# Kernel optimization log

Hardware: AMD Instinct MI355X
Metric: run time of the kernel (lower is better)

The kernel has to match this reference:

```python
import jax, jax.numpy as jnp
import numpy as np

B, T, D, H = 4, 2048, 1024, 16
HD = D // H  # head_dim = 64


def setup_inputs() -> dict:
    key = jax.random.key(0)
    k1, k2, k3, k4, k5 = jax.random.split(key, 5)
    scale = 1.0 / np.sqrt(D)
    return {
        "x": jax.random.normal(k1, (B, T, D), dtype=jnp.float32),
        "mask": jnp.ones((B, T), dtype=jnp.int32),
        "W_qkv": jax.random.normal(k2, (D, 3 * D), dtype=jnp.float32) * scale,
        "b_qkv": jax.random.normal(k3, (3 * D,), dtype=jnp.float32) * 0.01,
        "W_out": jax.random.normal(k4, (D, D), dtype=jnp.float32) * scale,
        "b_out": jax.random.normal(k5, (D,), dtype=jnp.float32) * 0.01,
    }


def reference(x, mask, W_qkv, b_qkv, W_out, b_out):
    Bx, Tx, Dm = x.shape
    qkv = x @ W_qkv + b_qkv                      # [B,T,3D]
    qkv = qkv.reshape(Bx, Tx, 3, H, HD)
    qkv = jnp.transpose(qkv, (2, 0, 3, 1, 4))    # [3,B,H,T,hd]
    q, k, v = qkv[0], qkv[1], qkv[2]
    att = jnp.einsum("bhqd,bhkd->bhqk", q, k) / jnp.sqrt(jnp.float32(HD))
    m = (mask[:, None, None, :] == 0)            # [B,1,1,T]
    att = jnp.where(m, jnp.float32(-1e9), att)
    att = jax.nn.softmax(att, axis=-1)
    out = jnp.einsum("bhqk,bhkd->bhqd", att, v)  # [B,H,T,hd]
    out = jnp.transpose(out, (0, 2, 1, 3)).reshape(Bx, Tx, Dm)
    return out @ W_out + b_out
```

## Files before the change

kernel.cpp:

```cpp
#include <hip/hip_runtime.h>
#include <hip/hip_bf16.h>
#include <stdint.h>

#define B_  4
#define T_  2048
#define D_  1024
#define H_  16
#define HD_ 64

typedef short s16x8 __attribute__((ext_vector_type(8)));
typedef short s16x4 __attribute__((ext_vector_type(4)));
typedef float f32x4 __attribute__((ext_vector_type(4)));

#define MFMA32(a, b, c) __builtin_amdgcn_mfma_f32_16x16x32_bf16(a, b, c, 0, 0, 0)

#if __has_builtin(__builtin_amdgcn_exp2f)
#define FEXP2(x) __builtin_amdgcn_exp2f(x)
#else
#define FEXP2(x) exp2f(x)
#endif

__device__ __forceinline__ unsigned short f2bf(float f) {
    union { float f; unsigned int u; } v; v.f = f;
    unsigned int r = v.u + 0x7fffu + ((v.u >> 16) & 1u);
    return (unsigned short)(r >> 16);
}

__device__ __forceinline__ unsigned int pkbf(float a, float b) {
    __hip_bfloat162 h = __float22bfloat162_rn(float2{a, b});
    union { __hip_bfloat162 h; unsigned int u; } v; v.h = h;
    return v.u;
}

__device__ __forceinline__ void async16(const void* g, void* l) {
    __builtin_amdgcn_global_load_lds(
        (const __attribute__((address_space(1))) unsigned int*)g,
        (__attribute__((address_space(3))) unsigned int*)l, 16, 0, 0);
}

__global__ __launch_bounds__(256)
void prep_kernel(const float* __restrict__ x, unsigned short* __restrict__ xb,
                 const float* __restrict__ Wq, unsigned short* __restrict__ Wqt,
                 const float* __restrict__ Wo, unsigned short* __restrict__ Wot) {
    const int blk = blockIdx.x;
    const int tid = threadIdx.x;
    if (blk < 8192) {
        const int i = blk * 256 + tid;
        float4 v = ((const float4*)x)[i];
        ushort4 o;
        o.x = f2bf(v.x); o.y = f2bf(v.y); o.z = f2bf(v.z); o.w = f2bf(v.w);
        ((ushort4*)xb)[i] = o;
        return;
    }
    __shared__ float t[32][33];
    const float* W; unsigned short* Wt; int K, N, bx, by;
    if (blk < 11264) {
        const int idx = blk - 8192;
        W = Wq; Wt = Wqt; K = 1024; N = 3072;
        bx = (idx % 96) * 32; by = (idx / 96) * 32;
    } else {
        const int idx = blk - 11264;
        W = Wo; Wt = Wot; K = 1024; N = 1024;
        bx = (idx % 32) * 32; by = (idx / 32) * 32;
    }
    const int tx = tid & 31, ty = tid >> 5;
    #pragma unroll
    for (int j = 0; j < 32; j += 8)
        t[ty + j][tx] = W[(size_t)(by + ty + j) * N + bx + tx];
    __syncthreads();
    #pragma unroll
    for (int j = 0; j < 32; j += 8)
        Wt[(size_t)(bx + ty + j) * K + by + tx] = f2bf(t[tx][ty + j]);
}

template <int MODE>
__global__ __launch_bounds__(256)
void gemm_bt_kernel(const unsigned short* __restrict__ A,
                    const unsigned short* __restrict__ Bt,
                    const float* __restrict__ bias,
                    float* __restrict__ Cf,
                    unsigned short* __restrict__ Qo,
                    unsigned short* __restrict__ Ko,
                    unsigned short* __restrict__ Vo,
                    int M, int N, int K) {
    __shared__ __align__(16) unsigned short SMEM[4 * 128 * 64];
    const int tid = threadIdx.x;
    const int w = tid >> 6, lane = tid & 63;
    const int laneN = lane & 15, quad = lane >> 4;
    const int rm0 = blockIdx.x * 128;
    const int rn0 = blockIdx.y * 128;
    const int wr = (w >> 1) * 64, wc = (w & 1) * 64;

    f32x4 acc[4][4] = {};

    auto issueG = [&](int kk, int bufsel) {
        unsigned short* As = SMEM + bufsel * 8192;
        unsigned short* Bs = SMEM + 16384 + bufsel * 8192;
        #pragma unroll
        for (int i = 0; i < 4; ++i) {
            const int c = i * 256 + tid;
            const int row = c >> 3, s = c & 7, g = s ^ (row & 7);
            async16(A + (size_t)(rm0 + row) * K + kk + g * 8,
                    (char*)As + (size_t)c * 16);
        }
        #pragma unroll
        for (int i = 0; i < 4; ++i) {
            const int c = i * 256 + tid;
            const int row = c >> 3, s = c & 7, g = s ^ (row & 7);
            async16(Bt + (size_t)(rn0 + row) * K + kk + g * 8,
                    (char*)Bs + (size_t)c * 16);
        }
    };

    issueG(0, 0);
    const int KI = K >> 6;
    for (int it = 0; it < KI; ++it) {
        const int buf = it & 1;
        __syncthreads();
        const unsigned short* As = SMEM + buf * 8192;
        const unsigned short* Bs = SMEM + 16384 + buf * 8192;
        s16x8 av[2][4], bv[2][4];
        #pragma unroll
        for (int h = 0; h < 2; ++h) {
            #pragma unroll
            for (int ms = 0; ms < 4; ++ms) {
                const int row = wr + ms * 16 + laneN;
                av[h][ms] = *(const s16x8*)&As[row * 64 + ((h * 4 + quad) ^ (row & 7)) * 8];
            }
            #pragma unroll
            for (int ns = 0; ns < 4; ++ns) {
                const int row = wc + ns * 16 + laneN;
                bv[h][ns] = *(const s16x8*)&Bs[row * 64 + ((h * 4 + quad) ^ (row & 7)) * 8];
            }
        }
        if (it + 1 < KI) issueG((it + 1) << 6, buf ^ 1);
        #pragma unroll
        for (int ms = 0; ms < 4; ++ms)
            #pragma unroll
            for (int ns = 0; ns < 4; ++ns) {
                acc[ms][ns] = MFMA32(av[0][ms], bv[0][ns], acc[ms][ns]);
                acc[ms][ns] = MFMA32(av[1][ms], bv[1][ns], acc[ms][ns]);
            }
    }

    if (MODE == 0) {
        #pragma unroll
        for (int ms = 0; ms < 4; ++ms) {
            const int gm0 = rm0 + wr + ms * 16 + quad * 4;
            #pragma unroll
            for (int ns = 0; ns < 4; ++ns) {
                const int gn = rn0 + wc + ns * 16 + laneN;
                const float bb = bias[gn];
                #pragma unroll
                for (int r = 0; r < 4; ++r)
                    Cf[(size_t)(gm0 + r) * N + gn] = acc[ms][ns][r] + bb;
            }
        }
    } else {
        const int s = rn0 >> 10;
        const int bidx = rm0 >> 11, t0 = rm0 & (T_ - 1);
        if (s < 2) {
            const float fs = (s == 0) ? 0.125f * 1.44269504088896f : 1.0f;
            unsigned short* P = (s == 0) ? Qo : Ko;
            #pragma unroll
            for (int ms = 0; ms < 4; ++ms) {
                const int lm0 = wr + ms * 16 + quad * 4;
                #pragma unroll
                for (int ns = 0; ns < 4; ++ns) {
                    const int gn = rn0 + wc + ns * 16 + laneN;
                    const float bb = bias[gn];
                    const int rr = gn & 1023, hh = rr >> 6, dd = rr & 63;
                    const size_t base = ((size_t)(bidx * H_ + hh) * T_ + t0);
                    #pragma unroll
                    for (int r = 0; r < 4; ++r)
                        P[(base + lm0 + r) * HD_ + dd] =
                            f2bf((acc[ms][ns][r] + bb) * fs);
                }
            }
        } else {
            __syncthreads();
            #pragma unroll
            for (int ms = 0; ms < 4; ++ms) {
                const int lm0 = wr + ms * 16 + quad * 4;
                #pragma unroll
                for (int ns = 0; ns < 4; ++ns) {
                    const int nl = wc + ns * 16 + laneN;
                    const float bb = bias[rn0 + nl];
                    const int sw = (nl & 7) << 3;
                    #pragma unroll
                    for (int r = 0; r < 4; ++r)
                        SMEM[nl * 128 + ((lm0 + r) ^ sw)] =
                            f2bf(acc[ms][ns][r] + bb);
                }
            }
            __syncthreads();
            const int nl = tid >> 1, half = tid & 1;
            const int hh = nl >> 6, d = nl & 63;
            const int hAbs = bidx * H_ + ((rn0 & 1023) >> 6) + hh;
            unsigned short* rowp = Vo + ((size_t)hAbs * HD_ + d) * T_ + t0;
            const int swz = nl & 7;
            #pragma unroll
            for (int j = 0; j < 8; ++j) {
                const s16x8 vv = *(const s16x8*)&SMEM[nl * 128 + half * 64 + j * 8];
                const int mlog = half * 64 + ((j ^ swz) * 8);
                *(s16x8*)(rowp + mlog) = vv;
            }
        }
    }
}

__global__ __launch_bounds__(512, 4)
void attn_kernel(const unsigned short* __restrict__ Q,
                 const unsigned short* __restrict__ Kb,
                 const unsigned short* __restrict__ VT,
                 const int* __restrict__ mask,
                 unsigned short* __restrict__ Out) {
    __shared__ __align__(16) unsigned short Ks[2][64 * 64];
    __shared__ __align__(16) unsigned short Vs[2][64 * 64];
    __shared__ float biasF[T_];
    const int tid = threadIdx.x;
    const int lane = tid & 63;
    const int w = tid >> 6;
    const int laneN = lane & 15, quad = lane >> 4;
    const int x7 = laneN & 7;
    const int bh = blockIdx.x;
    const int b = bh >> 4, h = bh & 15;
    const int qbase = blockIdx.y * 256 + w * 32;

    for (int i = tid; i < T_; i += 512)
        biasF[i] = mask[b * T_ + i] ? 0.f : -1.0e9f;

    s16x8 qf[2][2];
    #pragma unroll
    for (int qg = 0; qg < 2; ++qg) {
        const size_t qoff = ((size_t)bh * T_ + qbase + qg * 16 + laneN) * HD_ + quad * 8;
        qf[qg][0] = *(const s16x8*)&Q[qoff];
        qf[qg][1] = *(const s16x8*)&Q[qoff + 32];
    }

    s16x8 ones;
    #pragma unroll
    for (int j = 0; j < 8; ++j) ones[j] = (short)0x3F80;

    const size_t kRow0 = (size_t)bh * T_ * HD_;
    const size_t vRow0 = (size_t)bh * HD_ * T_;

    auto issueTile = [&](int kt, int bufsel) {
        const int kbase = kt * 64;
        {
            const int c = tid;
            const int row = c >> 3, s = c & 7;
            const int fk = (row & 3) | (((row >> 3) & 1) << 2);
            const int g = s ^ fk;
            async16(Kb + kRow0 + (size_t)(kbase + row) * HD_ + g * 8,
                    &Ks[bufsel][c * 8]);
        }
        {
            const int c = tid;
            const int d = c >> 3, s = c & 7, g = s ^ (d & 7);
            async16(VT + vRow0 + (size_t)d * T_ + kbase + g * 8,
                    &Vs[bufsel][c * 8]);
        }
    };

    issueTile(0, 0);

    f32x4 O[2][4] = {};
    f32x4 liacc[2] = {};

    const int rowA = ((laneN >> 2) << 3) + (laneN & 3);

    #pragma unroll 2
    for (int kt = 0; kt < T_ / 64; ++kt) {
        const int buf = kt & 1;
        const int kbase = kt * 64;
        __syncthreads();
        if (kt + 1 < T_ / 64) issueTile(kt + 1, buf ^ 1);

        s16x8 pf[2][2];
        #pragma unroll
        for (int g32 = 0; g32 < 2; ++g32) {
            const int ra = g32 * 32 + rowA;
            const s16x8 kA0 = *(const s16x8*)&Ks[buf][(ra * 8 + (quad ^ x7)) * 8];
            const s16x8 kA1 = *(const s16x8*)&Ks[buf][(ra * 8 + ((4 + quad) ^ x7)) * 8];
            const s16x8 kB0 = *(const s16x8*)&Ks[buf][((ra + 4) * 8 + (quad ^ x7)) * 8];
            const s16x8 kB1 = *(const s16x8*)&Ks[buf][((ra + 4) * 8 + ((4 + quad) ^ x7)) * 8];
            const f32x4 bA = *(const f32x4*)&biasF[kbase + g32 * 32 + quad * 8];
            const f32x4 bB = *(const f32x4*)&biasF[kbase + g32 * 32 + quad * 8 + 4];
            #pragma unroll
            for (int qg = 0; qg < 2; ++qg) {
                f32x4 Sa = bA, Sb = bB;
                Sa = MFMA32(kA0, qf[qg][0], Sa);
                Sa = MFMA32(kA1, qf[qg][1], Sa);
                Sb = MFMA32(kB0, qf[qg][0], Sb);
                Sb = MFMA32(kB1, qf[qg][1], Sb);
                #pragma unroll
                for (int r = 0; r < 4; ++r) {
                    Sa[r] = FEXP2(Sa[r]);
                    Sb[r] = FEXP2(Sb[r]);
                }
                union { s16x8 v; unsigned int u[4]; } pu;
                pu.u[0] = pkbf(Sa[0], Sa[1]);
                pu.u[1] = pkbf(Sa[2], Sa[3]);
                pu.u[2] = pkbf(Sb[0], Sb[1]);
                pu.u[3] = pkbf(Sb[2], Sb[3]);
                pf[qg][g32] = pu.v;
            }
        }

        #pragma unroll
        for (int g32 = 0; g32 < 2; ++g32) {
            s16x8 vf[4];
            #pragma unroll
            for (int nt = 0; nt < 4; ++nt) {
                const int d = nt * 16 + laneN;
                vf[nt] = *(const s16x8*)&Vs[buf][(d * 8 + ((g32 * 4 + quad) ^ x7)) * 8];
            }
            #pragma unroll
            for (int qg = 0; qg < 2; ++qg) {
                #pragma unroll
                for (int nt = 0; nt < 4; ++nt)
                    O[qg][nt] = MFMA32(pf[qg][g32], vf[nt], O[qg][nt]);
                liacc[qg] = MFMA32(pf[qg][g32], ones, liacc[qg]);
            }
        }
    }

    #pragma unroll
    for (int qg = 0; qg < 2; ++qg) {
        #pragma unroll
        for (int r = 0; r < 4; ++r) {
            const float inv = 1.0f / liacc[qg][r];
            const int tq = qbase + qg * 16 + quad * 4 + r;
            #pragma unroll
            for (int nt = 0; nt < 4; ++nt)
                Out[(size_t)(b * T_ + tq) * D_ + h * HD_ + nt * 16 + laneN] =
                    f2bf(O[qg][nt][r] * inv);
        }
    }
}

extern "C" void kernel_launch(void* const* d_in, const int* in_sizes, int n_in,
                              void* d_out, int out_size, void* d_ws, size_t ws_size,
                              hipStream_t stream) {
    const float* x     = (const float*)d_in[0];
    const int*   mask  = (const int*)d_in[1];
    const float* W_qkv = (const float*)d_in[2];
    const float* b_qkv = (const float*)d_in[3];
    const float* W_out = (const float*)d_in[4];
    const float* b_out = (const float*)d_in[5];
    float* out = (float*)d_out;

    unsigned short* ws = (unsigned short*)d_ws;
    const size_t NX = (size_t)B_ * T_ * D_;
    unsigned short* xb  = ws;
    unsigned short* Qb  = xb + NX;
    unsigned short* Kb  = Qb + NX;
    unsigned short* Vtb = Kb + NX;
    unsigned short* Wqt = Vtb + NX;
    unsigned short* Wot = Wqt + (size_t)3 * D_ * D_;
    unsigned short* attn = xb;

    prep_kernel<<<12288, 256, 0, stream>>>(x, xb, W_qkv, Wqt, W_out, Wot);
    gemm_bt_kernel<1><<<dim3(B_ * T_ / 128, 3 * D_ / 128), 256, 0, stream>>>(
        xb, Wqt, b_qkv, nullptr, Qb, Kb, Vtb, B_ * T_, 3 * D_, D_);
    attn_kernel<<<dim3(B_ * H_, T_ / 256), 512, 0, stream>>>(Qb, Kb, Vtb, mask, attn);
    gemm_bt_kernel<0><<<dim3(B_ * T_ / 128, D_ / 128), 256, 0, stream>>>(
        attn, Wot, b_out, out, nullptr, nullptr, nullptr, B_ * T_, D_, D_);
}
```

Baseline: 247.3 us.

## Add 256x256-tile QKV GEMM kernel with 512 threads and double-buffered async loads

Replaces the 128x128-tile QKV projection GEMM with a dedicated kernel using 256x256 output tiles, 8 waves, swizzled LDS double-buffering via async global-to-LDS copies, and setprio around MFMA bursts. Larger tiles raise arithmetic intensity and cut global/L2 traffic per FLOP. The V-transpose epilogue is adapted to the wider tile. In exchange it uses 128KB LDS and many accumulator registers per block, which lowers occupancy, and the grid shrinks to 384 blocks, which may under-fill the GPU.

```diff
diff --git a/kernel.cpp b/kernel.cpp
--- a/kernel.cpp
+++ b/kernel.cpp
@@ -156,55 +156,153 @@
                     Cf[(size_t)(gm0 + r) * N + gn] = acc[ms][ns][r] + bb;
             }
         }
+    }
+}
+
+__global__ __launch_bounds__(512, 2)
+void gemm256_qkv_kernel(const unsigned short* __restrict__ A,
+                        const unsigned short* __restrict__ Bt,
+                        const float* __restrict__ bias,
+                        unsigned short* __restrict__ Qo,
+                        unsigned short* __restrict__ Ko,
+                        unsigned short* __restrict__ Vo,
+                        int M, int N, int K) {
+    __shared__ __align__(16) unsigned short SMEM[65536];
+    const int tid = threadIdx.x;
+    const int w = tid >> 6, lane = tid & 63;
+    const int laneN = lane & 15, quad = lane >> 4;
+    const int wm = w >> 2, wn = w & 3;
+    const int rm0 = blockIdx.x * 256;
+    const int rn0 = blockIdx.y * 256;
+
+    f32x4 acc[8][4] = {};
+
+    auto issueTile = [&](int kk, int bufsel) {
+        unsigned short* As = SMEM + bufsel * 16384;
+        unsigned short* Bs = SMEM + 32768 + bufsel * 16384;
+        #pragma unroll
+        for (int i = 0; i < 4; ++i) {
+            const int c = i * 512 + tid;
+            const int row = c >> 3, s = c & 7, g = s ^ (row & 7);
+            async16(A + (size_t)(rm0 + row) * K + kk + g * 8,
+                    (char*)As + (size_t)c * 16);
+        }
+        #pragma unroll
+        for (int i = 0; i < 4; ++i) {
+            const int c = i * 512 + tid;
+            const int row = c >> 3, s = c & 7, g = s ^ (row & 7);
+            async16(Bt + (size_t)(rn0 + row) * K + kk + g * 8,
+                    (char*)Bs + (size_t)c * 16);
+        }
+    };
+
+    issueTile(0, 0);
+    issueTile(64, 1);
+    asm volatile("s_waitcnt vmcnt(8)" ::: "memory");
+    __builtin_amdgcn_s_barrier();
+    asm volatile("" ::: "memory");
+
+    const int KI = K >> 6;
+    #pragma unroll 2
+    for (int kt = 0; kt < KI; ++kt) {
+        const int buf = kt & 1;
+        const unsigned short* As = SMEM + buf * 16384;
+        const unsigned short* Bs = SMEM + 32768 + buf * 16384;
+        s16x8 av[4], bv[4];
+        #pragma unroll
+        for (int kh = 0; kh < 2; ++kh) {
+            #pragma unroll
+            for (int ns = 0; ns < 4; ++ns) {
+                const int row = wn * 64 + ns * 16 + laneN;
+                bv[ns] = *(const s16x8*)&Bs[row * 64 + ((kh * 4 + quad) ^ (row & 7)) * 8];
+            }
+            #pragma unroll
+            for (int ms = 0; ms < 4; ++ms) {
+                const int row = wm * 128 + ms * 16 + laneN;
+                av[ms] = *(const s16x8*)&As[row * 64 + ((kh * 4 + quad) ^ (row & 7)) * 8];
+            }
+            __builtin_amdgcn_s_setprio(1);
+            #pragma unroll
+            for (int ms = 0; ms < 4; ++ms)
+                #pragma unroll
+                for (int ns = 0; ns < 4; ++ns)
+                    acc[ms][ns] = MFMA32(av[ms], bv[ns], acc[ms][ns]);
+            __builtin_amdgcn_s_setprio(0);
+            #pragma unroll
+            for (int ms = 0; ms < 4; ++ms) {
+                const int row = wm * 128 + 64 + ms * 16 + laneN;
+                av[ms] = *(const s16x8*)&As[row * 64 + ((kh * 4 + quad) ^ (row & 7)) * 8];
+            }
+            __builtin_amdgcn_s_setprio(1);
+            #pragma unroll
+            for (int ms = 0; ms < 4; ++ms)
+                #pragma unroll
+                for (int ns = 0; ns < 4; ++ns)
+                    acc[4 + ms][ns] = MFMA32(av[ms], bv[ns], acc[4 + ms][ns]);
+            __builtin_amdgcn_s_setprio(0);
+        }
+        __builtin_amdgcn_s_barrier();
+        asm volatile("" ::: "memory");
+        if (kt + 2 < KI) {
+            issueTile((kt + 2) << 6, buf);
+            asm volatile("s_waitcnt vmcnt(8)" ::: "memory");
+        } else if (kt + 1 < KI) {
+            asm volatile("s_waitcnt vmcnt(0)" ::: "memory");
+        }
+        if (kt + 1 < KI) {
+            __builtin_amdgcn_s_barrier();
+            asm volatile("" ::: "memory");
+        }
+    }
+
+    const int s = rn0 >> 10;
+    const int bidx = rm0 >> 11, t0 = rm0 & (T_ - 1);
+    if (s < 2) {
+        const float fs = (s == 0) ? 0.125f * 1.44269504088896f : 1.0f;
+        unsigned short* P = (s == 0) ? Qo : Ko;
+        #pragma unroll
+        for (int a = 0; a < 8; ++a) {
+            const int lm0 = wm * 128 + (a >> 2) * 64 + (a & 3) * 16 + quad * 4;
+            #pragma unroll
+            for (int ns = 0; ns < 4; ++ns) {
+                const int gn = rn0 + wn * 64 + ns * 16 + laneN;
+                const float bb = bias[gn];
+                const int rr = gn & 1023, hh = rr >> 6, dd = rr & 63;
+                const size_t base = ((size_t)(bidx * H_ + hh) * T_ + t0);
+                #pragma unroll
+                for (int r = 0; r < 4; ++r)
+                    P[(base + lm0 + r) * HD_ + dd] =
+                        f2bf((acc[a][ns][r] + bb) * fs);
+            }
+        }
     } else {
-        const int s = rn0 >> 10;
-        const int bidx = rm0 >> 11, t0 = rm0 & (T_ - 1);
-        if (s < 2) {
-            const float fs = (s == 0) ? 0.125f * 1.44269504088896f : 1.0f;
-            unsigned short* P = (s == 0) ? Qo : Ko;
-            #pragma unroll
-            for (int ms = 0; ms < 4; ++ms) {
-                const int lm0 = wr + ms * 16 + quad * 4;
-                #pragma unroll
-                for (int ns = 0; ns < 4; ++ns) {
-                    const int gn = rn0 + wc + ns * 16 + laneN;
-                    const float bb = bias[gn];
-                    const int rr = gn & 1023, hh = rr >> 6, dd = rr & 63;
-                    const size_t base = ((size_t)(bidx * H_ + hh) * T_ + t0);
-                    #pragma unroll
-                    for (int r = 0; r < 4; ++r)
-                        P[(base + lm0 + r) * HD_ + dd] =
-                            f2bf((acc[ms][ns][r] + bb) * fs);
-                }
-            }
-        } else {
-            __syncthreads();
-            #pragma unroll
-            for (int ms = 0; ms < 4; ++ms) {
-                const int lm0 = wr + ms * 16 + quad * 4;
-                #pragma unroll
-                for (int ns = 0; ns < 4; ++ns) {
-                    const int nl = wc + ns * 16 + laneN;
-                    const float bb = bias[rn0 + nl];
-                    const int sw = (nl & 7) << 3;
-                    #pragma unroll
-                    for (int r = 0; r < 4; ++r)
-                        SMEM[nl * 128 + ((lm0 + r) ^ sw)] =
-                            f2bf(acc[ms][ns][r] + bb);
-                }
-            }
-            __syncthreads();
-            const int nl = tid >> 1, half = tid & 1;
-            const int hh = nl >> 6, d = nl & 63;
-            const int hAbs = bidx * H_ + ((rn0 & 1023) >> 6) + hh;
-            unsigned short* rowp = Vo + ((size_t)hAbs * HD_ + d) * T_ + t0;
-            const int swz = nl & 7;
-            #pragma unroll
-            for (int j = 0; j < 8; ++j) {
-                const s16x8 vv = *(const s16x8*)&SMEM[nl * 128 + half * 64 + j * 8];
-                const int mlog = half * 64 + ((j ^ swz) * 8);
-                *(s16x8*)(rowp + mlog) = vv;
-            }
+        __syncthreads();
+        #pragma unroll
+        for (int a = 0; a < 8; ++a) {
+            const int lm0 = wm * 128 + (a >> 2) * 64 + (a & 3) * 16 + quad * 4;
+            #pragma unroll
+            for (int ns = 0; ns < 4; ++ns) {
+                const int nl = wn * 64 + ns * 16 + laneN;
+                const float bb = bias[rn0 + nl];
+                const int sw = (nl & 7) << 3;
+                #pragma unroll
+                for (int r = 0; r < 4; ++r)
+                    SMEM[nl * 256 + ((lm0 + r) ^ sw)] =
+                        f2bf(acc[a][ns][r] + bb);
+            }
+        }
+        __syncthreads();
+        const int nl = tid >> 1, half = tid & 1;
+        const int hh = nl >> 6, d = nl & 63;
+        const int hAbs = bidx * H_ + ((rn0 & 1023) >> 6) + hh;
+        unsigned short* rowp = Vo + ((size_t)hAbs * HD_ + d) * T_ + t0;
+        const int swz = nl & 7;
+        #pragma unroll
+        for (int j = 0; j < 16; ++j) {
+            const int mgl = half * 16 + j;
+            const int pg = (mgl & 24) | ((mgl & 7) ^ swz);
+            const s16x8 vv = *(const s16x8*)&SMEM[nl * 256 + pg * 8];
+            *(s16x8*)(rowp + mgl * 8) = vv;
         }
     }
 }
@@ -362,8 +460,8 @@
     unsigned short* attn = xb;
 
     prep_kernel<<<12288, 256, 0, stream>>>(x, xb, W_qkv, Wqt, W_out, Wot);
-    gemm_bt_kernel<1><<<dim3(B_ * T_ / 128, 3 * D_ / 128), 256, 0, stream>>>(
-        xb, Wqt, b_qkv, nullptr, Qb, Kb, Vtb, B_ * T_, 3 * D_, D_);
+    gemm256_qkv_kernel<<<dim3(B_ * T_ / 256, 3 * D_ / 256), 512, 0, stream>>>(
+        xb, Wqt, b_qkv, Qb, Kb, Vtb, B_ * T_, 3 * D_, D_);
     attn_kernel<<<dim3(B_ * H_, T_ / 256), 512, 0, stream>>>(Qb, Kb, Vtb, mask, attn);
     gemm_bt_kernel<0><<<dim3(B_ * T_ / 128, D_ / 128), 256, 0, stream>>>(
         attn, Wot, b_out, out, nullptr, nullptr, nullptr, B_ * T_, D_, D_);
```

Measured after the change: 264.0 us. 6.8% more time.

## Use 128-key tiles, fuse QK and PV per chunk, add MFMA priority hints

Applied to the files above, without the earlier changes.

Doubles the K/V tile per iteration from 64 to 128 keys, which halves the number of __syncthreads barriers and async-copy rounds. The QK^T, exp and PV stages are merged per 32-key chunk, so P fragments are consumed right away instead of being buffered. s_setprio is raised around the MFMA groups to favour matrix issue across waves. Doubled LDS (about 72KB per block) may lower occupancy against the launch bound of 4 blocks, and the V swizzle changes to a 16-slot layout.

```diff
diff --git a/kernel.cpp b/kernel.cpp
--- a/kernel.cpp
+++ b/kernel.cpp
@@ -215,8 +215,8 @@
                  const unsigned short* __restrict__ VT,
                  const int* __restrict__ mask,
                  unsigned short* __restrict__ Out) {
-    __shared__ __align__(16) unsigned short Ks[2][64 * 64];
-    __shared__ __align__(16) unsigned short Vs[2][64 * 64];
+    __shared__ __align__(16) unsigned short Ks[2][128 * 64];
+    __shared__ __align__(16) unsigned short Vs[2][64 * 128];
     __shared__ float biasF[T_];
     const int tid = threadIdx.x;
     const int lane = tid & 63;
@@ -246,18 +246,21 @@
     const size_t vRow0 = (size_t)bh * HD_ * T_;
 
     auto issueTile = [&](int kt, int bufsel) {
-        const int kbase = kt * 64;
-        {
-            const int c = tid;
+        const int kbase = kt * 128;
+        #pragma unroll
+        for (int i = 0; i < 2; ++i) {
+            const int c = i * 512 + tid;
             const int row = c >> 3, s = c & 7;
             const int fk = (row & 3) | (((row >> 3) & 1) << 2);
             const int g = s ^ fk;
             async16(Kb + kRow0 + (size_t)(kbase + row) * HD_ + g * 8,
                     &Ks[bufsel][c * 8]);
         }
-        {
-            const int c = tid;
-            const int d = c >> 3, s = c & 7, g = s ^ (d & 7);
+        #pragma unroll
+        for (int i = 0; i < 2; ++i) {
+            const int c = i * 512 + tid;
+            const int d = c >> 4, s = c & 15;
+            const int g = (s & 8) | ((s & 7) ^ (d & 7));
             async16(VT + vRow0 + (size_t)d * T_ + kbase + g * 8,
                     &Vs[bufsel][c * 8]);
         }
@@ -270,30 +273,39 @@
 
     const int rowA = ((laneN >> 2) << 3) + (laneN & 3);
 
+    const int NT = T_ / 128;
     #pragma unroll 2
-    for (int kt = 0; kt < T_ / 64; ++kt) {
+    for (int kt = 0; kt < NT; ++kt) {
         const int buf = kt & 1;
-        const int kbase = kt * 64;
+        const int kbase = kt * 128;
         __syncthreads();
-        if (kt + 1 < T_ / 64) issueTile(kt + 1, buf ^ 1);
-
-        s16x8 pf[2][2];
-        #pragma unroll
-        for (int g32 = 0; g32 < 2; ++g32) {
+        if (kt + 1 < NT) issueTile(kt + 1, buf ^ 1);
+
+        #pragma unroll
+        for (int g32 = 0; g32 < 4; ++g32) {
             const int ra = g32 * 32 + rowA;
             const s16x8 kA0 = *(const s16x8*)&Ks[buf][(ra * 8 + (quad ^ x7)) * 8];
             const s16x8 kA1 = *(const s16x8*)&Ks[buf][(ra * 8 + ((4 + quad) ^ x7)) * 8];
             const s16x8 kB0 = *(const s16x8*)&Ks[buf][((ra + 4) * 8 + (quad ^ x7)) * 8];
             const s16x8 kB1 = *(const s16x8*)&Ks[buf][((ra + 4) * 8 + ((4 + quad) ^ x7)) * 8];
+            s16x8 vf[4];
+            const int jslot = g32 * 4 + quad;
+            #pragma unroll
+            for (int nt = 0; nt < 4; ++nt) {
+                const int d = nt * 16 + laneN;
+                vf[nt] = *(const s16x8*)&Vs[buf][(d * 16 + (jslot ^ x7)) * 8];
+            }
             const f32x4 bA = *(const f32x4*)&biasF[kbase + g32 * 32 + quad * 8];
             const f32x4 bB = *(const f32x4*)&biasF[kbase + g32 * 32 + quad * 8 + 4];
             #pragma unroll
             for (int qg = 0; qg < 2; ++qg) {
                 f32x4 Sa = bA, Sb = bB;
+                __builtin_amdgcn_s_setprio(1);
                 Sa = MFMA32(kA0, qf[qg][0], Sa);
                 Sa = MFMA32(kA1, qf[qg][1], Sa);
                 Sb = MFMA32(kB0, qf[qg][0], Sb);
                 Sb = MFMA32(kB1, qf[qg][1], Sb);
+                __builtin_amdgcn_s_setprio(0);
                 #pragma unroll
                 for (int r = 0; r < 4; ++r) {
                     Sa[r] = FEXP2(Sa[r]);
@@ -304,24 +316,12 @@
                 pu.u[1] = pkbf(Sa[2], Sa[3]);
                 pu.u[2] = pkbf(Sb[0], Sb[1]);
                 pu.u[3] = pkbf(Sb[2], Sb[3]);
-                pf[qg][g32] = pu.v;
-            }
-        }
-
-        #pragma unroll
-        for (int g32 = 0; g32 < 2; ++g32) {
-            s16x8 vf[4];
-            #pragma unroll
-            for (int nt = 0; nt < 4; ++nt) {
-                const int d = nt * 16 + laneN;
-                vf[nt] = *(const s16x8*)&Vs[buf][(d * 8 + ((g32 * 4 + quad) ^ x7)) * 8];
-            }
-            #pragma unroll
-            for (int qg = 0; qg < 2; ++qg) {
+                __builtin_amdgcn_s_setprio(1);
                 #pragma unroll
                 for (int nt = 0; nt < 4; ++nt)
-                    O[qg][nt] = MFMA32(pf[qg][g32], vf[nt], O[qg][nt]);
-                liacc[qg] = MFMA32(pf[qg][g32], ones, liacc[qg]);
+                    O[qg][nt] = MFMA32(pu.v, vf[nt], O[qg][nt]);
+                liacc[qg] = MFMA32(pu.v, ones, liacc[qg]);
+                __builtin_amdgcn_s_setprio(0);
             }
         }
     }
```

Measured after the change: 308.2 us. 1.25x slower.
